# Kernel tuning notes

Measured on AMD Instinct MI355X. Metric: run time of the kernel, lower is better.

Reference implementation:

```python
import jax, jax.numpy as jnp
import numpy as np

N = 100000   # nodes
E = 1600000  # edges (avg degree 16)
D = 32       # feature dim

def setup_inputs() -> dict:
    key = jax.random.key(0)
    k1, k2, k3, k4 = jax.random.split(key, 4)
    feat = jax.random.normal(k1, (N, D), dtype=jnp.float32)
    e_feat = jax.random.normal(k2, (E, 1), dtype=jnp.float32)
    src = jax.random.randint(k3, (E,), 0, N)
    dst = jax.random.randint(k4, (E,), 0, N)
    return {"feat": feat, "e_feat": e_feat, "src": src, "dst": dst}

def reference(feat, e_feat, src, dst):
    n = feat.shape[0]
    ones = jnp.ones(src.shape[0], dtype=feat.dtype)
    # degrees computed on the full graph (before self-loop removal), as in DGL code
    out_deg = jax.ops.segment_sum(ones, src, num_segments=n)
    in_deg = jax.ops.segment_sum(ones, dst, num_segments=n)
    src_norm = jnp.power(jnp.clip(out_deg, 1.0, None), -0.5)[:, None]  # [N,1]
    dst_norm = jnp.power(jnp.clip(in_deg, 1.0, None), -0.5)[:, None]   # [N,1]
    # remove_self_loop: mask out self-loop edges in the aggregation only
    mask = (src != dst).astype(feat.dtype)[:, None]                    # [E,1]
    # u_mul_e: gather normalized src features, multiply by edge weight
    msg = (feat * src_norm)[src] * (e_feat * mask)                     # [E,D]
    agg = jax.ops.segment_sum(msg, dst, num_segments=n)                # [N,D]
    out = feat - agg * dst_norm
    return jnp.sum(jnp.abs(out), axis=1)                               # [N]
```

## Files before the change

### kernel.cpp

```cpp
#include <hip/hip_runtime.h>

#define D 32
#define RANGE 128
#define RMAX 800
#define JC 512
#define CHUNKMAX 3200
#define CAP 2304

__global__ __launch_bounds__(512) void sort_chunks(
        const int* __restrict__ src, const int* __restrict__ dst,
        const float* __restrict__ ef,
        uint2* __restrict__ recs, unsigned* __restrict__ recsS,
        unsigned* __restrict__ metaD, unsigned* __restrict__ metaS,
        int E, int R, int chunk) {
    __shared__ uint2 sd[CHUNKMAX];
    __shared__ unsigned ss_[CHUNKMAX];
    __shared__ int cd[RMAX], cs[RMAX];
    __shared__ int curD[RMAX], curS[RMAX];
    int j = blockIdx.x, t = threadIdx.x;
    int e0 = j * chunk, e1 = min(E, e0 + chunk), cntE = e1 - e0;
    for (int i = t; i < RMAX; i += 512) { cd[i] = 0; cs[i] = 0; }
    __syncthreads();
    for (int e = e0 + 2 * t; e < e1; e += 1024) {
        if (e + 1 < e1) {
            int2 s2 = *(const int2*)(src + e);
            int2 d2 = *(const int2*)(dst + e);
            atomicAdd(&cd[d2.x >> 7], 1);
            atomicAdd(&cd[d2.y >> 7], 1);
            atomicAdd(&cs[s2.x >> 7], 1);
            atomicAdd(&cs[s2.y >> 7], 1);
        } else {
            atomicAdd(&cd[dst[e] >> 7], 1);
            atomicAdd(&cs[src[e] >> 7], 1);
        }
    }
    __syncthreads();
    {
        int i1 = t + 512;
        curD[t] = cd[t]; curS[t] = cs[t];
        if (i1 < RMAX) { curD[i1] = cd[i1]; curS[i1] = cs[i1]; }
        __syncthreads();
        for (int off = 1; off < RMAX; off <<= 1) {
            int vD0 = (t >= off) ? curD[t - off] : 0;
            int vS0 = (t >= off) ? curS[t - off] : 0;
            int vD1 = 0, vS1 = 0;
            if (i1 < RMAX && i1 >= off) { vD1 = curD[i1 - off]; vS1 = curS[i1 - off]; }
            __syncthreads();
            curD[t] += vD0; curS[t] += vS0;
            if (i1 < RMAX) { curD[i1] += vD1; curS[i1] += vS1; }
            __syncthreads();
        }
        curD[t] -= cd[t]; curS[t] -= cs[t];
        if (i1 < RMAX) { curD[i1] -= cd[i1]; curS[i1] -= cs[i1]; }
        __syncthreads();
    }
    for (int e = e0 + t; e < e1; e += 512) {
        int s = src[e], d = dst[e];
        float w = (s == d) ? 0.0f : ef[e];
        int pos = atomicAdd(&curD[d >> 7], 1);
        sd[pos] = make_uint2((unsigned)s | ((unsigned)(d & (RANGE - 1)) << 17),
                             __float_as_uint(w));
        int ps = atomicAdd(&curS[s >> 7], 1);
        ss_[ps] = (unsigned)s;
    }
    __syncthreads();
    size_t baseE = (size_t)j * chunk;
    for (int i = t; i < cntE; i += 512) {
        recs[baseE + i] = sd[i];
        recsS[baseE + i] = ss_[i];
    }
    for (int i = t; i < R; i += 512) {
        metaD[(size_t)j * R + i] = ((unsigned)(curD[i] - cd[i]) << 16) | (unsigned)cd[i];
        metaS[(size_t)j * R + i] = ((unsigned)(curS[i] - cs[i]) << 16) | (unsigned)cs[i];
    }
}

__device__ __forceinline__ unsigned short f2bf(float x) {
    unsigned u = __float_as_uint(x);
    u += 0x7FFFu + ((u >> 16) & 1u);
    return (unsigned short)(u >> 16);
}

__global__ __launch_bounds__(512) void srcnorm_convert(
        const unsigned* __restrict__ recsS, const unsigned* __restrict__ metaS,
        const float* __restrict__ feat, unsigned short* __restrict__ featb,
        int n, int R, int chunk) {
    __shared__ int cnt[RANGE];
    int r = blockIdx.x, t = threadIdx.x;
    int base = r * RANGE, lim = min(n - base, RANGE);
    if (t < RANGE) cnt[t] = 0;
    __syncthreads();
    unsigned m = metaS[(size_t)t * R + r];
    int st = m >> 16, c = m & 0xFFFFu;
    const unsigned* p = recsS + (size_t)t * chunk + st;
    for (int k = 0; k < c; k++) atomicAdd(&cnt[p[k] - (unsigned)base], 1);
    __syncthreads();
    int total4 = lim * 8;
    for (int i = t; i < total4; i += 512) {
        int row = i >> 3;
        float sn = rsqrtf((float)max(cnt[row], 1));
        float4 f = ((const float4*)(feat + (size_t)(base + row) * D))[i & 7];
        ushort4 u;
        u.x = f2bf(f.x * sn); u.y = f2bf(f.y * sn);
        u.z = f2bf(f.z * sn); u.w = f2bf(f.w * sn);
        ((ushort4*)(featb + (size_t)(base + row) * D))[i & 7] = u;
    }
}

__global__ __launch_bounds__(512) void gather_kernel(
        const float* __restrict__ feat, const unsigned short* __restrict__ featb,
        const uint2* __restrict__ recs, const unsigned* __restrict__ metaD,
        float* __restrict__ out, int n, int R, int chunk) {
    __shared__ uint2 raw[CAP];
    __shared__ uint2 srec[CAP];
    __shared__ int segpre[JC + 1];
    __shared__ int indeg[RANGE];
    __shared__ int pre[RANGE + 1];
    int r = blockIdx.x, t = threadIdx.x;
    int base = r * RANGE, lim = min(n - base, RANGE);
    unsigned m = metaD[(size_t)t * R + r];
    int st = m >> 16, c = m & 0xFFFFu;
    segpre[t + 1] = c;
    if (t == 0) segpre[0] = 0;
    if (t < RANGE) indeg[t] = 0;
    __syncthreads();
    for (int off = 1; off < JC; off <<= 1) {
        int v = (t + 1 > off) ? segpre[t + 1 - off] : 0;
        __syncthreads();
        segpre[t + 1] += v;
        __syncthreads();
    }
    int total = segpre[JC];
    bool ovf = total > CAP;
    const uint2* p = recs + (size_t)t * chunk + st;
    if (!ovf) {
        int dp = segpre[t];
        for (int k = 0; k < c; k++) {
            uint2 rec = p[k];
            raw[dp + k] = rec;
            atomicAdd(&indeg[rec.x >> 17], 1);
        }
    } else {
        for (int k = 0; k < c; k++) atomicAdd(&indeg[p[k].x >> 17], 1);
    }
    __syncthreads();
    if (t < RANGE) pre[t + 1] = indeg[t];
    if (t == 0) pre[0] = 0;
    __syncthreads();
    for (int off = 1; off < RANGE; off <<= 1) {
        int v = 0;
        if (t < RANGE) { int idx = t + 1; if (idx > off) v = pre[idx - off]; }
        __syncthreads();
        if (t < RANGE) pre[t + 1] += v;
        __syncthreads();
    }
    if (t < RANGE) indeg[t] = pre[t];
    __syncthreads();
    if (!ovf) {
        for (int i = t; i < total; i += 512) {
            uint2 rec = raw[i];
            int dl = rec.x >> 17;
            int pos = atomicAdd(&indeg[dl], 1);
            srec[pos] = make_uint2(rec.x & 0x1FFFFu, rec.y);
        }
    }
    __syncthreads();
    int node = t >> 2;
    int cch = t & 3;
    if (node >= lim) return;
    int p0i = pre[node];
    int cnt = pre[node + 1] - p0i;
    float a0 = 0.f, a1 = 0.f, a2 = 0.f, a3 = 0.f, a4 = 0.f, a5 = 0.f, a6 = 0.f, a7 = 0.f;
    if (!ovf) {
        const uint2* sp = srec + p0i;
        int i = 0;
        for (; i + 4 <= cnt; i += 4) {
            uint2 q0 = sp[i], q1 = sp[i + 1], q2 = sp[i + 2], q3 = sp[i + 3];
            uint4 b0 = ((const uint4*)(featb + (size_t)q0.x * D))[cch];
            uint4 b1 = ((const uint4*)(featb + (size_t)q1.x * D))[cch];
            uint4 b2 = ((const uint4*)(featb + (size_t)q2.x * D))[cch];
            uint4 b3 = ((const uint4*)(featb + (size_t)q3.x * D))[cch];
            float w0 = __uint_as_float(q0.y), w1 = __uint_as_float(q1.y);
            float w2 = __uint_as_float(q2.y), w3 = __uint_as_float(q3.y);
            a0 += __uint_as_float(b0.x << 16) * w0 + __uint_as_float(b1.x << 16) * w1
                + __uint_as_float(b2.x << 16) * w2 + __uint_as_float(b3.x << 16) * w3;
            a1 += __uint_as_float(b0.x & 0xFFFF0000u) * w0 + __uint_as_float(b1.x & 0xFFFF0000u) * w1
                + __uint_as_float(b2.x & 0xFFFF0000u) * w2 + __uint_as_float(b3.x & 0xFFFF0000u) * w3;
            a2 += __uint_as_float(b0.y << 16) * w0 + __uint_as_float(b1.y << 16) * w1
                + __uint_as_float(b2.y << 16) * w2 + __uint_as_float(b3.y << 16) * w3;
            a3 += __uint_as_float(b0.y & 0xFFFF0000u) * w0 + __uint_as_float(b1.y & 0xFFFF0000u) * w1
                + __uint_as_float(b2.y & 0xFFFF0000u) * w2 + __uint_as_float(b3.y & 0xFFFF0000u) * w3;
            a4 += __uint_as_float(b0.z << 16) * w0 + __uint_as_float(b1.z << 16) * w1
                + __uint_as_float(b2.z << 16) * w2 + __uint_as_float(b3.z << 16) * w3;
            a5 += __uint_as_float(b0.z & 0xFFFF0000u) * w0 + __uint_as_float(b1.z & 0xFFFF0000u) * w1
                + __uint_as_float(b2.z & 0xFFFF0000u) * w2 + __uint_as_float(b3.z & 0xFFFF0000u) * w3;
            a6 += __uint_as_float(b0.w << 16) * w0 + __uint_as_float(b1.w << 16) * w1
                + __uint_as_float(b2.w << 16) * w2 + __uint_as_float(b3.w << 16) * w3;
            a7 += __uint_as_float(b0.w & 0xFFFF0000u) * w0 + __uint_as_float(b1.w & 0xFFFF0000u) * w1
                + __uint_as_float(b2.w & 0xFFFF0000u) * w2 + __uint_as_float(b3.w & 0xFFFF0000u) * w3;
        }
        for (; i < cnt; i++) {
            uint2 q = sp[i];
            uint4 b = ((const uint4*)(featb + (size_t)q.x * D))[cch];
            float w = __uint_as_float(q.y);
            a0 += __uint_as_float(b.x << 16) * w;
            a1 += __uint_as_float(b.x & 0xFFFF0000u) * w;
            a2 += __uint_as_float(b.y << 16) * w;
            a3 += __uint_as_float(b.y & 0xFFFF0000u) * w;
            a4 += __uint_as_float(b.z << 16) * w;
            a5 += __uint_as_float(b.z & 0xFFFF0000u) * w;
            a6 += __uint_as_float(b.w << 16) * w;
            a7 += __uint_as_float(b.w & 0xFFFF0000u) * w;
        }
    } else {
        for (int j = 0; j < JC; j++) {
            unsigned mm = metaD[(size_t)j * R + r];
            const uint2* pp = recs + (size_t)j * chunk + (mm >> 16);
            int cc = mm & 0xFFFFu;
            for (int k = 0; k < cc; k++) {
                uint2 rec = pp[k];
                if ((int)(rec.x >> 17) == node) {
                    uint4 b = ((const uint4*)(featb + (size_t)(rec.x & 0x1FFFFu) * D))[cch];
                    float w = __uint_as_float(rec.y);
                    a0 += __uint_as_float(b.x << 16) * w;
                    a1 += __uint_as_float(b.x & 0xFFFF0000u) * w;
                    a2 += __uint_as_float(b.y << 16) * w;
                    a3 += __uint_as_float(b.y & 0xFFFF0000u) * w;
                    a4 += __uint_as_float(b.z << 16) * w;
                    a5 += __uint_as_float(b.z & 0xFFFF0000u) * w;
                    a6 += __uint_as_float(b.w << 16) * w;
                    a7 += __uint_as_float(b.w & 0xFFFF0000u) * w;
                }
            }
        }
    }
    float dn = rsqrtf((float)max(cnt, 1));
    const float4* fr = (const float4*)(feat + (size_t)(base + node) * D);
    float4 fA = fr[cch * 2];
    float4 fB = fr[cch * 2 + 1];
    float v = fabsf(fA.x - a0 * dn) + fabsf(fA.y - a1 * dn) +
              fabsf(fA.z - a2 * dn) + fabsf(fA.w - a3 * dn) +
              fabsf(fB.x - a4 * dn) + fabsf(fB.y - a5 * dn) +
              fabsf(fB.z - a6 * dn) + fabsf(fB.w - a7 * dn);
    v += __shfl_xor(v, 1, 4);
    v += __shfl_xor(v, 2, 4);
    if (cch == 0) out[base + node] = v;
}

extern "C" void kernel_launch(void* const* d_in, const int* in_sizes, int n_in,
                              void* d_out, int out_size, void* d_ws, size_t ws_size,
                              hipStream_t stream) {
    const float* feat   = (const float*)d_in[0];
    const float* e_feat = (const float*)d_in[1];
    const int*   src    = (const int*)d_in[2];
    const int*   dst    = (const int*)d_in[3];
    const int E = in_sizes[2];
    const int n = in_sizes[0] / D;
    float* out = (float*)d_out;

    const int R = (n + RANGE - 1) / RANGE;
    const int chunk = (((E + JC - 1) / JC) + 1) & ~1;

    char* p = (char*)d_ws;
    uint2* recs    = (uint2*)p;    p += ((size_t)JC * chunk * 8 + 15) & ~(size_t)15;
    unsigned* recsS = (unsigned*)p; p += ((size_t)JC * chunk * 4 + 15) & ~(size_t)15;
    unsigned* metaD = (unsigned*)p; p += ((size_t)JC * R * 4 + 15) & ~(size_t)15;
    unsigned* metaS = (unsigned*)p; p += ((size_t)JC * R * 4 + 15) & ~(size_t)15;
    unsigned short* featb = (unsigned short*)p;

    sort_chunks<<<JC, 512, 0, stream>>>(src, dst, e_feat, recs, recsS, metaD, metaS,
                                        E, R, chunk);

    srcnorm_convert<<<R, 512, 0, stream>>>(recsS, metaS, feat, featb, n, R, chunk);

    gather_kernel<<<R, 512, 0, stream>>>(feat, featb, recs, metaD, out, n, R, chunk);
}
```

Measured before the change: 144.8 us.

## Split bf16 feature table into two halves gathered in separate passes

Stores the bf16-converted normalized features as two half-width tables (first 16 and last 16 features) and runs the per-node gather loop twice, once per half. The goal is a smaller working set per pass that stays resident in L2 during the random source gathers. In exchange the edge records in shared memory are read twice and each gather issues narrower 8-byte loads, doubling load instruction count.

```diff
diff --git a/kernel.cpp b/kernel.cpp
--- a/kernel.cpp
+++ b/kernel.cpp
@@ -83,7 +83,8 @@
 
 __global__ __launch_bounds__(512) void srcnorm_convert(
         const unsigned* __restrict__ recsS, const unsigned* __restrict__ metaS,
-        const float* __restrict__ feat, unsigned short* __restrict__ featb,
+        const float* __restrict__ feat,
+        unsigned short* __restrict__ featbA, unsigned short* __restrict__ featbB,
         int n, int R, int chunk) {
     __shared__ int cnt[RANGE];
     int r = blockIdx.x, t = threadIdx.x;
@@ -98,17 +99,20 @@
     int total4 = lim * 8;
     for (int i = t; i < total4; i += 512) {
         int row = i >> 3;
+        int ch = i & 7;
         float sn = rsqrtf((float)max(cnt[row], 1));
-        float4 f = ((const float4*)(feat + (size_t)(base + row) * D))[i & 7];
+        float4 f = ((const float4*)(feat + (size_t)(base + row) * D))[ch];
         ushort4 u;
         u.x = f2bf(f.x * sn); u.y = f2bf(f.y * sn);
         u.z = f2bf(f.z * sn); u.w = f2bf(f.w * sn);
-        ((ushort4*)(featb + (size_t)(base + row) * D))[i & 7] = u;
+        unsigned short* tbl = (ch < 4) ? featbA : featbB;
+        ((ushort4*)(tbl + (size_t)(base + row) * 16))[ch & 3] = u;
     }
 }
 
 __global__ __launch_bounds__(512) void gather_kernel(
-        const float* __restrict__ feat, const unsigned short* __restrict__ featb,
+        const float* __restrict__ feat,
+        const unsigned short* __restrict__ featbA, const unsigned short* __restrict__ featbB,
         const uint2* __restrict__ recs, const unsigned* __restrict__ metaD,
         float* __restrict__ out, int n, int R, int chunk) {
     __shared__ uint2 raw[CAP];
@@ -176,10 +180,10 @@
         int i = 0;
         for (; i + 4 <= cnt; i += 4) {
             uint2 q0 = sp[i], q1 = sp[i + 1], q2 = sp[i + 2], q3 = sp[i + 3];
-            uint4 b0 = ((const uint4*)(featb + (size_t)q0.x * D))[cch];
-            uint4 b1 = ((const uint4*)(featb + (size_t)q1.x * D))[cch];
-            uint4 b2 = ((const uint4*)(featb + (size_t)q2.x * D))[cch];
-            uint4 b3 = ((const uint4*)(featb + (size_t)q3.x * D))[cch];
+            uint2 b0 = ((const uint2*)(featbA + (size_t)q0.x * 16))[cch];
+            uint2 b1 = ((const uint2*)(featbA + (size_t)q1.x * 16))[cch];
+            uint2 b2 = ((const uint2*)(featbA + (size_t)q2.x * 16))[cch];
+            uint2 b3 = ((const uint2*)(featbA + (size_t)q3.x * 16))[cch];
             float w0 = __uint_as_float(q0.y), w1 = __uint_as_float(q1.y);
             float w2 = __uint_as_float(q2.y), w3 = __uint_as_float(q3.y);
             a0 += __uint_as_float(b0.x << 16) * w0 + __uint_as_float(b1.x << 16) * w1
@@ -190,27 +194,42 @@
                 + __uint_as_float(b2.y << 16) * w2 + __uint_as_float(b3.y << 16) * w3;
             a3 += __uint_as_float(b0.y & 0xFFFF0000u) * w0 + __uint_as_float(b1.y & 0xFFFF0000u) * w1
                 + __uint_as_float(b2.y & 0xFFFF0000u) * w2 + __uint_as_float(b3.y & 0xFFFF0000u) * w3;
-            a4 += __uint_as_float(b0.z << 16) * w0 + __uint_as_float(b1.z << 16) * w1
-                + __uint_as_float(b2.z << 16) * w2 + __uint_as_float(b3.z << 16) * w3;
-            a5 += __uint_as_float(b0.z & 0xFFFF0000u) * w0 + __uint_as_float(b1.z & 0xFFFF0000u) * w1
-                + __uint_as_float(b2.z & 0xFFFF0000u) * w2 + __uint_as_float(b3.z & 0xFFFF0000u) * w3;
-            a6 += __uint_as_float(b0.w << 16) * w0 + __uint_as_float(b1.w << 16) * w1
-                + __uint_as_float(b2.w << 16) * w2 + __uint_as_float(b3.w << 16) * w3;
-            a7 += __uint_as_float(b0.w & 0xFFFF0000u) * w0 + __uint_as_float(b1.w & 0xFFFF0000u) * w1
-                + __uint_as_float(b2.w & 0xFFFF0000u) * w2 + __uint_as_float(b3.w & 0xFFFF0000u) * w3;
         }
         for (; i < cnt; i++) {
             uint2 q = sp[i];
-            uint4 b = ((const uint4*)(featb + (size_t)q.x * D))[cch];
+            uint2 b = ((const uint2*)(featbA + (size_t)q.x * 16))[cch];
             float w = __uint_as_float(q.y);
             a0 += __uint_as_float(b.x << 16) * w;
             a1 += __uint_as_float(b.x & 0xFFFF0000u) * w;
             a2 += __uint_as_float(b.y << 16) * w;
             a3 += __uint_as_float(b.y & 0xFFFF0000u) * w;
-            a4 += __uint_as_float(b.z << 16) * w;
-            a5 += __uint_as_float(b.z & 0xFFFF0000u) * w;
-            a6 += __uint_as_float(b.w << 16) * w;
-            a7 += __uint_as_float(b.w & 0xFFFF0000u) * w;
+        }
+        i = 0;
+        for (; i + 4 <= cnt; i += 4) {
+            uint2 q0 = sp[i], q1 = sp[i + 1], q2 = sp[i + 2], q3 = sp[i + 3];
+            uint2 b0 = ((const uint2*)(featbB + (size_t)q0.x * 16))[cch];
+            uint2 b1 = ((const uint2*)(featbB + (size_t)q1.x * 16))[cch];
+            uint2 b2 = ((const uint2*)(featbB + (size_t)q2.x * 16))[cch];
+            uint2 b3 = ((const uint2*)(featbB + (size_t)q3.x * 16))[cch];
+            float w0 = __uint_as_float(q0.y), w1 = __uint_as_float(q1.y);
+            float w2 = __uint_as_float(q2.y), w3 = __uint_as_float(q3.y);
+            a4 += __uint_as_float(b0.x << 16) * w0 + __uint_as_float(b1.x << 16) * w1
+                + __uint_as_float(b2.x << 16) * w2 + __uint_as_float(b3.x << 16) * w3;
+            a5 += __uint_as_float(b0.x & 0xFFFF0000u) * w0 + __uint_as_float(b1.x & 0xFFFF0000u) * w1
+                + __uint_as_float(b2.x & 0xFFFF0000u) * w2 + __uint_as_float(b3.x & 0xFFFF0000u) * w3;
+            a6 += __uint_as_float(b0.y << 16) * w0 + __uint_as_float(b1.y << 16) * w1
+                + __uint_as_float(b2.y << 16) * w2 + __uint_as_float(b3.y << 16) * w3;
+            a7 += __uint_as_float(b0.y & 0xFFFF0000u) * w0 + __uint_as_float(b1.y & 0xFFFF0000u) * w1
+                + __uint_as_float(b2.y & 0xFFFF0000u) * w2 + __uint_as_float(b3.y & 0xFFFF0000u) * w3;
+        }
+        for (; i < cnt; i++) {
+            uint2 q = sp[i];
+            uint2 b = ((const uint2*)(featbB + (size_t)q.x * 16))[cch];
+            float w = __uint_as_float(q.y);
+            a4 += __uint_as_float(b.x << 16) * w;
+            a5 += __uint_as_float(b.x & 0xFFFF0000u) * w;
+            a6 += __uint_as_float(b.y << 16) * w;
+            a7 += __uint_as_float(b.y & 0xFFFF0000u) * w;
         }
     } else {
         for (int j = 0; j < JC; j++) {
@@ -220,24 +239,26 @@
             for (int k = 0; k < cc; k++) {
                 uint2 rec = pp[k];
                 if ((int)(rec.x >> 17) == node) {
-                    uint4 b = ((const uint4*)(featb + (size_t)(rec.x & 0x1FFFFu) * D))[cch];
+                    unsigned sidx = rec.x & 0x1FFFFu;
+                    uint2 bA = ((const uint2*)(featbA + (size_t)sidx * 16))[cch];
+                    uint2 bB = ((const uint2*)(featbB + (size_t)sidx * 16))[cch];
                     float w = __uint_as_float(rec.y);
-                    a0 += __uint_as_float(b.x << 16) * w;
-                    a1 += __uint_as_float(b.x & 0xFFFF0000u) * w;
-                    a2 += __uint_as_float(b.y << 16) * w;
-                    a3 += __uint_as_float(b.y & 0xFFFF0000u) * w;
-                    a4 += __uint_as_float(b.z << 16) * w;
-                    a5 += __uint_as_float(b.z & 0xFFFF0000u) * w;
-                    a6 += __uint_as_float(b.w << 16) * w;
-                    a7 += __uint_as_float(b.w & 0xFFFF0000u) * w;
+                    a0 += __uint_as_float(bA.x << 16) * w;
+                    a1 += __uint_as_float(bA.x & 0xFFFF0000u) * w;
+                    a2 += __uint_as_float(bA.y << 16) * w;
+                    a3 += __uint_as_float(bA.y & 0xFFFF0000u) * w;
+                    a4 += __uint_as_float(bB.x << 16) * w;
+                    a5 += __uint_as_float(bB.x & 0xFFFF0000u) * w;
+                    a6 += __uint_as_float(bB.y << 16) * w;
+                    a7 += __uint_as_float(bB.y & 0xFFFF0000u) * w;
                 }
             }
         }
     }
     float dn = rsqrtf((float)max(cnt, 1));
     const float4* fr = (const float4*)(feat + (size_t)(base + node) * D);
-    float4 fA = fr[cch * 2];
-    float4 fB = fr[cch * 2 + 1];
+    float4 fA = fr[cch];
+    float4 fB = fr[cch + 4];
     float v = fabsf(fA.x - a0 * dn) + fabsf(fA.y - a1 * dn) +
               fabsf(fA.z - a2 * dn) + fabsf(fA.w - a3 * dn) +
               fabsf(fB.x - a4 * dn) + fabsf(fB.y - a5 * dn) +
@@ -266,12 +287,13 @@
     unsigned* recsS = (unsigned*)p; p += ((size_t)JC * chunk * 4 + 15) & ~(size_t)15;
     unsigned* metaD = (unsigned*)p; p += ((size_t)JC * R * 4 + 15) & ~(size_t)15;
     unsigned* metaS = (unsigned*)p; p += ((size_t)JC * R * 4 + 15) & ~(size_t)15;
-    unsigned short* featb = (unsigned short*)p;
+    unsigned short* featbA = (unsigned short*)p; p += ((size_t)n * 16 * 2 + 15) & ~(size_t)15;
+    unsigned short* featbB = (unsigned short*)p;
 
     sort_chunks<<<JC, 512, 0, stream>>>(src, dst, e_feat, recs, recsS, metaD, metaS,
                                         E, R, chunk);
 
-    srcnorm_convert<<<R, 512, 0, stream>>>(recsS, metaS, feat, featb, n, R, chunk);
-
-    gather_kernel<<<R, 512, 0, stream>>>(feat, featb, recs, metaD, out, n, R, chunk);
-}
+    srcnorm_convert<<<R, 512, 0, stream>>>(recsS, metaS, feat, featbA, featbB, n, R, chunk);
+
+    gather_kernel<<<R, 512, 0, stream>>>(feat, featbA, featbB, recs, metaD, out, n, R, chunk);
+}
```

Measured after the change: 151.7 us. +4.8%, slower.
